# Kernel optimization log

Measured on AMD Instinct MI355X. Metric: run time of the kernel, lower is better.

## Reference

```python
import jax, jax.numpy as jnp
import numpy as np

B, N = 32, 128
V, P, L = 50000, 40, 50
WD, UD = 100, 25
D = WD + UD          # 125: LSTM hidden per direction
H2 = 2 * D           # 250: BiLSTM output
HID = 100            # hidden_dim for scorers


def setup_inputs() -> dict:
    key = jax.random.key(0)
    ks = iter(jax.random.split(key, 40))
    p = lambda shape: jax.random.normal(next(ks), shape, jnp.float32) * 0.05
    inp = {
        'word_ids': jax.random.randint(next(ks), (B, N), 0, V),
        'upos_ids': jax.random.randint(next(ks), (B, N), 0, P),
        'target_arcs': jax.random.randint(next(ks), (B, N), 0, N),
        'wlookup': p((V, WD)),
        'tlookup': p((V, UD)),  # original sizes tag table by word_count
        # LSTM layer 0 (input D=125), layer 1 (input 2D=250); f=fwd, b=bwd dir
        'l0f_Wih': p((4 * D, D)), 'l0f_Whh': p((4 * D, D)), 'l0f_b': p((4 * D,)),
        'l0b_Wih': p((4 * D, D)), 'l0b_Whh': p((4 * D, D)), 'l0b_b': p((4 * D,)),
        'l1f_Wih': p((4 * D, H2)), 'l1f_Whh': p((4 * D, D)), 'l1f_b': p((4 * D,)),
        'l1b_Wih': p((4 * D, H2)), 'l1b_Whh': p((4 * D, D)), 'l1b_b': p((4 * D,)),
        'eh_W': p((HID, H2)), 'eh_b': p((HID,)),
        'em_W': p((HID, H2)), 'em_b': p((HID,)),
        'es_W': p((1, HID)), 'es_b': p((1,)),
        'lh_W': p((HID, H2)), 'lh_b': p((HID,)),
        'lm_W': p((HID, H2)), 'lm_b': p((HID,)),
        'ls_W': p((L, HID)), 'ls_b': p((L,)),
    }
    return inp


def _lstm_dir(x, Wih, Whh, b, reverse):
    # x: [B,T,in] -> h: [B,T,H], pytorch gate order i,f,g,o
    H = Whh.shape[1]
    xg = jnp.einsum('bti,gi->btg', x, Wih) + b  # precompute input projections

    def step(carry, xt):
        h, c = carry
        g = xt + h @ Whh.T
        i, f, gg, o = jnp.split(g, 4, axis=-1)
        c = jax.nn.sigmoid(f) * c + jax.nn.sigmoid(i) * jnp.tanh(gg)
        h = jax.nn.sigmoid(o) * jnp.tanh(c)
        return (h, c), h

    h0 = jnp.zeros((x.shape[0], H), x.dtype)
    _, hs = jax.lax.scan(step, (h0, h0), jnp.swapaxes(xg, 0, 1), reverse=reverse)
    return jnp.swapaxes(hs, 0, 1)


def _bilstm(x, Wf, Uf, bf, Wb, Ub, bb):
    return jnp.concatenate([_lstm_dir(x, Wf, Uf, bf, False),
                            _lstm_dir(x, Wb, Ub, bb, True)], axis=-1)


def reference(word_ids, upos_ids, target_arcs, wlookup, tlookup,
              l0f_Wih, l0f_Whh, l0f_b, l0b_Wih, l0b_Whh, l0b_b,
              l1f_Wih, l1f_Whh, l1f_b, l1b_Wih, l1b_Whh, l1b_b,
              eh_W, eh_b, em_W, em_b, es_W, es_b,
              lh_W, lh_b, lm_W, lm_b, ls_W, ls_b):
    n = word_ids.shape[1]
    words = jnp.concatenate([wlookup[word_ids], tlookup[upos_ids]], axis=-1)  # [B,N,125]
    h0 = _bilstm(words, l0f_Wih, l0f_Whh, l0f_b, l0b_Wih, l0b_Whh, l0b_b)
    word_exprs = _bilstm(h0, l1f_Wih, l1f_Whh, l1f_b, l1b_Wih, l1b_Whh, l1b_b)  # [B,N,250]

    word_h = word_exprs @ eh_W.T + eh_b  # [B,N,100]
    word_m = word_exprs @ em_W.T + em_b
    # fused pairwise biaffine-style scoring (replaces the O(n) python loop)
    pair = jnp.tanh(word_h[:, :, None, :] + word_m[:, None, :, :])  # [B,N,N,100]
    arc_scores = jnp.einsum('bijh,h->bij', pair, es_W[0]) + es_b[0]  # [B,N,N]

    # training path: margin augmentation
    target_arcs = target_arcs.at[:, 0].set(0)
    margin = 1.0 - jax.nn.one_hot(target_arcs, n, dtype=arc_scores.dtype)
    arc_scores = arc_scores + margin

    # decode() is an external MST decoder; greedy argmax stand-in
    parsed_trees = jnp.argmax(arc_scores, axis=-1)

    tree = target_arcs  # is_train path
    rel_heads = jnp.take_along_axis(word_exprs, tree[:, :, None], axis=1)  # [B,N,250]
    rel_heads = rel_heads @ lh_W.T + lh_b
    rel_mod = word_exprs @ lm_W.T + lm_b
    rel_scores = jnp.tanh(rel_mod + rel_heads) @ ls_W.T + ls_b  # [B,N,L]
    predicted_rels = jnp.argmax(rel_scores, axis=-1)
    return (parsed_trees, predicted_rels, arc_scores, rel_scores)
```

## Files before the change

kernel.cpp:

```cpp
#include <hip/hip_runtime.h>
#include <hip/hip_bf16.h>
#include <math.h>

#define B 32
#define N 128
#define BT (B*N)
#define WD 100
#define UD 25
#define D 125
#define G4 (4*D)
#define H2 (2*D)
#define HID 100
#define L 50

__device__ __forceinline__ float fast_tanh(float x) {
    float e = __expf(2.0f * x);
    return 1.0f - 2.0f / (e + 1.0f);
}
__device__ __forceinline__ float fast_sigmoid(float x) {
    return 1.0f / (1.0f + __expf(-x));
}
__device__ __forceinline__ float bcast_lane(float v, int k) {
    return __builtin_bit_cast(float, __builtin_amdgcn_readlane(__builtin_bit_cast(int, v), k));
}

#define REP64(X) \
 X(0) X(1) X(2) X(3) X(4) X(5) X(6) X(7) X(8) X(9) \
 X(10) X(11) X(12) X(13) X(14) X(15) X(16) X(17) X(18) X(19) \
 X(20) X(21) X(22) X(23) X(24) X(25) X(26) X(27) X(28) X(29) \
 X(30) X(31) X(32) X(33) X(34) X(35) X(36) X(37) X(38) X(39) \
 X(40) X(41) X(42) X(43) X(44) X(45) X(46) X(47) X(48) X(49) \
 X(50) X(51) X(52) X(53) X(54) X(55) X(56) X(57) X(58) X(59) \
 X(60) X(61) X(62) X(63)

__global__ void bias_setup(const float* __restrict__ l0f_b, const float* __restrict__ l0b_b,
                           const float* __restrict__ l1f_b, const float* __restrict__ l1b_b,
                           const float* __restrict__ eh_b, const float* __restrict__ em_b,
                           const float* __restrict__ lm_b,
                           float* __restrict__ b_l0, float* __restrict__ b_l1,
                           float* __restrict__ b_s3) {
    int t = blockIdx.x * blockDim.x + threadIdx.x;
    if (t < 500)        b_l0[t] = l0f_b[t];
    else if (t < 1000)  b_l0[t] = l0b_b[t-500];
    else if (t < 1500)  b_l1[t-1000] = l1f_b[t-1000];
    else if (t < 2000)  b_l1[t-1000] = l1b_b[t-1500];
    else if (t < 2100)  b_s3[t-2000] = eh_b[t-2000];
    else if (t < 2200)  b_s3[t-2000] = em_b[t-2100];
    else if (t < 2300)  b_s3[t-2000] = lm_b[t-2200];
}

__global__ void pad_zero(float* __restrict__ w0, float* __restrict__ w1,
                         float* __restrict__ w2, float* __restrict__ w3) {
    int t = blockIdx.x * blockDim.x + threadIdx.x;
    int m = t / 1516, e = t % 1516;
    float* p = (m == 0) ? w0 : (m == 1) ? w1 : (m == 2) ? w2 : w3;
    p[125*500 + e] = 0.0f;
}

struct TJob { const float* src; float* dst; int R, C, ldo, coff, tile0, tiles_x; };
struct TArgs { TJob j[12]; };

__global__ __launch_bounds__(256)
void transpose_fused(TArgs a) {
    int bid = blockIdx.x;
    int ji = 0;
    #pragma unroll
    for (int i = 1; i < 12; i++) if (bid >= a.j[i].tile0) ji = i;
    TJob jb = a.j[ji];
    int t = bid - jb.tile0;
    int tx = t % jb.tiles_x;
    int ty = t / jb.tiles_x;
    __shared__ float tile[32][33];
    int k0 = tx*32, n0 = ty*32;
    #pragma unroll
    for (int dy = 0; dy < 32; dy += 8) {
        int n = n0 + threadIdx.y + dy;
        int k = k0 + threadIdx.x;
        if (n < jb.R && k < jb.C)
            tile[threadIdx.y+dy][threadIdx.x] = jb.src[(size_t)n*jb.C + k];
    }
    __syncthreads();
    #pragma unroll
    for (int dy = 0; dy < 32; dy += 8) {
        int k = k0 + threadIdx.y + dy;
        int n = n0 + threadIdx.x;
        if (k < jb.C && n < jb.R)
            jb.dst[(size_t)k*jb.ldo + jb.coff + n] = tile[threadIdx.x][threadIdx.y+dy];
    }
}

__global__ void embed_kernel(const int* __restrict__ wids, const int* __restrict__ uids,
                             const float* __restrict__ wl, const float* __restrict__ tl,
                             float* __restrict__ words) {
    int bt = blockIdx.x;
    int t = threadIdx.x;
    int wid = wids[bt];
    int uid = uids[bt];
    if (t < WD)       words[bt*D + t] = wl[wid*WD + t];
    else if (t < D)   words[bt*D + t] = tl[uid*UD + (t - WD)];
}

#define MT 16
template<int CPT>
__global__ __launch_bounds__(512)
void proj_t(const float* __restrict__ x, const float* __restrict__ WT,
            const float* __restrict__ bias, float* __restrict__ out,
            int Ncols, int K, int ldx, const int* __restrict__ gather_idx) {
    __shared__ float xs[250 * 17 + 16];
    int m0 = blockIdx.x * MT;
    for (int e = threadIdx.x; e < MT * K; e += blockDim.x) {
        int r = e / K, k = e - r * K;
        int m = m0 + r;
        int row = m;
        if (gather_idx) {
            int bb = m >> 7, np = m & 127;
            row = (bb << 7) + (np == 0 ? 0 : gather_idx[m]);
        }
        xs[k*17 + r] = x[(size_t)row*ldx + k];
    }
    __syncthreads();
    int n0 = threadIdx.x;
    int lane = threadIdx.x & 63;
    int bd = blockDim.x;
    float acc[CPT][MT];
    int ncl[CPT];
    #pragma unroll
    for (int j = 0; j < CPT; j++) {
        int n = n0 + j*bd;
        ncl[j] = (n < Ncols) ? n : (Ncols - 1);
        #pragma unroll
        for (int r = 0; r < MT; r++) acc[j][r] = 0.0f;
    }
    float wkc[4][CPT];
    #pragma unroll
    for (int q = 0; q < 4; q++)
        #pragma unroll
        for (int j = 0; j < CPT; j++)
            wkc[q][j] = WT[(size_t)q*Ncols + ncl[j]];
    int k0 = 0;
    for (; k0 + 8 <= K; k0 += 4) {
        float xv = xs[(k0 + (lane >> 4))*17 + (lane & 15)];
        float wkn[4][CPT];
        #pragma unroll
        for (int q = 0; q < 4; q++)
            #pragma unroll
            for (int j = 0; j < CPT; j++)
                wkn[q][j] = WT[(size_t)(k0 + 4 + q)*Ncols + ncl[j]];
        #pragma unroll
        for (int q = 0; q < 4; q++) {
            #pragma unroll
            for (int r = 0; r < 16; r++) {
                float hv = bcast_lane(xv, q*16 + r);
                #pragma unroll
                for (int j = 0; j < CPT; j++)
                    acc[j][r] = fmaf(wkc[q][j], hv, acc[j][r]);
            }
        }
        #pragma unroll
        for (int q = 0; q < 4; q++)
            #pragma unroll
            for (int j = 0; j < CPT; j++)
                wkc[q][j] = wkn[q][j];
    }
    {
        float xv = xs[(k0 + (lane >> 4))*17 + (lane & 15)];
        #pragma unroll
        for (int q = 0; q < 4; q++) {
            #pragma unroll
            for (int r = 0; r < 16; r++) {
                float hv = bcast_lane(xv, q*16 + r);
                #pragma unroll
                for (int j = 0; j < CPT; j++)
                    acc[j][r] = fmaf(wkc[q][j], hv, acc[j][r]);
            }
        }
        k0 += 4;
    }
    for (; k0 < K; k0++) {
        float xv = xs[k0*17 + (lane & 15)];
        float wk[CPT];
        #pragma unroll
        for (int j = 0; j < CPT; j++) wk[j] = WT[(size_t)k0*Ncols + ncl[j]];
        #pragma unroll
        for (int r = 0; r < 16; r++) {
            float hv = bcast_lane(xv, r);
            #pragma unroll
            for (int j = 0; j < CPT; j++)
                acc[j][r] = fmaf(wk[j], hv, acc[j][r]);
        }
    }
    #pragma unroll
    for (int j = 0; j < CPT; j++) {
        int n = n0 + j*bd;
        if (n < Ncols) {
            float bb = bias[n];
            #pragma unroll
            for (int r = 0; r < MT; r++) out[(size_t)(m0 + r)*Ncols + n] = acc[j][r] + bb;
        }
    }
}

__global__ __launch_bounds__(1024, 4)
void lstm_scan(const float* __restrict__ xgc,
               const float* __restrict__ WhTf, const float* __restrict__ WhTb,
               float* __restrict__ out) {
    int dir = blockIdx.x & 1;
    int b = blockIdx.x >> 1;
    const float* WhT = dir ? WhTb : WhTf;
    int off = dir ? D : 0;
    int t = threadIdx.x;
    int g = t & 511;
    int half = t >> 9;
    int kbase = half << 6;

    __shared__ __align__(16) float hbuf[128];
    __shared__ float pbuf[1024];

    unsigned voff0 = ((unsigned)kbase * 500u + (unsigned)g) * 4u;
#define DECLW(i) float w##i; \
    asm volatile("global_load_dword %0, %1, %2" \
                 : "=v"(w##i) : "v"(voff0 + (unsigned)(i)*2000u), "s"(WhT));
    REP64(DECLW)
#undef DECLW
    asm volatile("s_waitcnt vmcnt(0)" ::: "memory");

    float c = 0.0f;
    if (t < 128) hbuf[t] = 0.0f;
    __syncthreads();

    const float* xb = xgc + (size_t)b * N * 1000 + dir * 500;
    bool xa = (half == 0) && (g < G4);
    float x_next = xa ? xb[(size_t)(dir ? (N-1) : 0) * 1000 + g] : 0.0f;

    const float4* h4q = ((const float4*)hbuf) + (kbase >> 2);

#define FMA4(q, i0, i1, i2, i3) { float4 hv = h4q[q]; \
    a4[0] = fmaf(w##i0, hv.x, a4[0]); \
    a4[1] = fmaf(w##i1, hv.y, a4[1]); \
    a4[2] = fmaf(w##i2, hv.z, a4[2]); \
    a4[3] = fmaf(w##i3, hv.w, a4[3]); }

    for (int ti = 0; ti < N; ti++) {
        int tt = dir ? (N-1-ti) : ti;
        float x_cur = x_next;
        float xn = 0.0f;
        if (xa && ti + 1 < N)
            xn = xb[(size_t)(dir ? (tt-1) : (tt+1)) * 1000 + g];
        float a4[4];
        a4[0] = x_cur; a4[1] = 0.0f; a4[2] = 0.0f; a4[3] = 0.0f;
        FMA4(0,  0,  1,  2,  3)  FMA4(1,  4,  5,  6,  7)
        FMA4(2,  8,  9, 10, 11)  FMA4(3, 12, 13, 14, 15)
        FMA4(4, 16, 17, 18, 19)  FMA4(5, 20, 21, 22, 23)
        FMA4(6, 24, 25, 26, 27)  FMA4(7, 28, 29, 30, 31)
        FMA4(8, 32, 33, 34, 35)  FMA4(9, 36, 37, 38, 39)
        FMA4(10, 40, 41, 42, 43) FMA4(11, 44, 45, 46, 47)
        FMA4(12, 48, 49, 50, 51) FMA4(13, 52, 53, 54, 55)
        FMA4(14, 56, 57, 58, 59) FMA4(15, 60, 61, 62, 63)
        x_next = xn;
        pbuf[t] = (a4[0] + a4[1]) + (a4[2] + a4[3]);
        __syncthreads();
        if (t < D) {
            float iv = pbuf[t]       + pbuf[512 + t];
            float fv = pbuf[D+t]     + pbuf[512 + D+t];
            float gv = pbuf[2*D+t]   + pbuf[512 + 2*D+t];
            float ov = pbuf[3*D+t]   + pbuf[512 + 3*D+t];
            float si = fast_sigmoid(iv);
            float sf = fast_sigmoid(fv);
            float so = fast_sigmoid(ov);
            c = sf * c + si * fast_tanh(gv);
            float h = so * fast_tanh(c);
            hbuf[t] = h;
            out[(size_t)(b*N + tt)*H2 + off + t] = h;
        }
        __syncthreads();
    }
#undef FMA4
}

#define ITILE 4
__global__ __launch_bounds__(128)
void arc_kernel(const float* __restrict__ s3,
                const float* __restrict__ esW, const float* __restrict__ esb,
                const int* __restrict__ ta,
                float* __restrict__ arc_out, float* __restrict__ tree_out) {
    int blk = blockIdx.x;
    int b = blk >> 5, it = blk & 31;
    int j = threadIdx.x;

    __shared__ float wms[128 * 101];
    __shared__ float whs[ITILE][HID];
    __shared__ float es[HID];
    __shared__ float sv[128];
    __shared__ int   si[128];

    for (int e = j; e < 128 * HID; e += 128) {
        int r = e / HID, h = e - r * HID;
        wms[r*101 + h] = s3[(size_t)(b*N + r)*300 + 100 + h];
    }
    for (int e = j; e < ITILE * HID; e += 128) {
        int ii = e / HID, h = e - ii * HID;
        whs[ii][h] = s3[(size_t)(b*N + it*ITILE + ii)*300 + h];
    }
    if (j < HID) es[j] = esW[j];
    __syncthreads();

    float eb = esb[0];
    const float* wmr = &wms[j * 101];
    for (int ii = 0; ii < ITILE; ii++) {
        int i = it * ITILE + ii;
        int bi = b * N + i;
        float acc = 0.0f;
        for (int h = 0; h < HID; h++)
            acc = fmaf(es[h], fast_tanh(whs[ii][h] + wmr[h]), acc);
        int tai = (i == 0) ? 0 : ta[bi];
        float score = acc + eb + 1.0f - ((j == tai) ? 1.0f : 0.0f);
        arc_out[(size_t)bi*N + j] = score;
        sv[j] = score; si[j] = j;
        __syncthreads();
        for (int s = 64; s; s >>= 1) {
            if (j < s) {
                float ov = sv[j+s]; int oi = si[j+s];
                if (ov > sv[j] || (ov == sv[j] && oi < si[j])) { sv[j] = ov; si[j] = oi; }
            }
            __syncthreads();
        }
        if (j == 0) tree_out[bi] = (float)si[0];
        __syncthreads();
    }
}

__global__ void rel_kernel(const float* __restrict__ s3, const float* __restrict__ rh,
                           const float* __restrict__ lsW, const float* __restrict__ lsb,
                           float* __restrict__ rel_out, float* __restrict__ pred_out) {
    int bt = blockIdx.x;
    int t = threadIdx.x;

    __shared__ float tv[HID];
    __shared__ float sv[64];
    __shared__ int   si[64];

    for (int h = t; h < HID; h += 64)
        tv[h] = fast_tanh(s3[(size_t)bt*300 + 200 + h] + rh[(size_t)bt*HID + h]);
    __syncthreads();

    float score = -1e30f;
    if (t < L) {
        float acc = 0.0f;
        const float* wrow = lsW + t*HID;
        for (int h = 0; h < HID; h++) acc = fmaf(wrow[h], tv[h], acc);
        score = acc + lsb[t];
        rel_out[(size_t)bt*L + t] = score;
    }
    sv[t] = score;
    si[t] = t;
    __syncthreads();
    for (int s = 32; s; s >>= 1) {
        if (t < s) {
            float ov = sv[t + s]; int oi = si[t + s];
            if (ov > sv[t] || (ov == sv[t] && oi < si[t])) { sv[t] = ov; si[t] = oi; }
        }
        __syncthreads();
    }
    if (t == 0) pred_out[bt] = (float)si[0];
}

extern "C" void kernel_launch(void* const* d_in, const int* in_sizes, int n_in,
                              void* d_out, int out_size, void* d_ws, size_t ws_size,
                              hipStream_t stream) {
    const int*   word_ids    = (const int*)  d_in[0];
    const int*   upos_ids    = (const int*)  d_in[1];
    const int*   target_arcs = (const int*)  d_in[2];
    const float* wlookup     = (const float*)d_in[3];
    const float* tlookup     = (const float*)d_in[4];
    const float* l0f_Wih = (const float*)d_in[5];
    const float* l0f_Whh = (const float*)d_in[6];
    const float* l0f_b   = (const float*)d_in[7];
    const float* l0b_Wih = (const float*)d_in[8];
    const float* l0b_Whh = (const float*)d_in[9];
    const float* l0b_b   = (const float*)d_in[10];
    const float* l1f_Wih = (const float*)d_in[11];
    const float* l1f_Whh = (const float*)d_in[12];
    const float* l1f_b   = (const float*)d_in[13];
    const float* l1b_Wih = (const float*)d_in[14];
    const float* l1b_Whh = (const float*)d_in[15];
    const float* l1b_b   = (const float*)d_in[16];
    const float* eh_W = (const float*)d_in[17];
    const float* eh_b = (const float*)d_in[18];
    const float* em_W = (const float*)d_in[19];
    const float* em_b = (const float*)d_in[20];
    const float* es_W = (const float*)d_in[21];
    const float* es_b = (const float*)d_in[22];
    const float* lh_W = (const float*)d_in[23];
    const float* lh_b = (const float*)d_in[24];
    const float* lm_W = (const float*)d_in[25];
    const float* lm_b = (const float*)d_in[26];
    const float* ls_W = (const float*)d_in[27];
    const float* ls_b = (const float*)d_in[28];

    float* out = (float*)d_out;
    float* trees_out = out;
    float* preds_out = out + BT;
    float* arc_out   = out + 2*BT;
    float* rel_out   = out + 2*BT + BT*N;

    float* ws = (float*)d_ws;
    float* A       = ws;
    float* words   = ws + 4096000;
    float* C       = ws + 4608000;
    float* WT_l0   = ws + 5632000;
    float* WT_l1   = ws + 5757000;
    float* WT_s3   = ws + 6007000;
    float* WT_lh   = ws + 6082000;
    float* WhT_l0f = ws + 6107000;
    float* WhT_l0b = ws + 6171016;
    float* WhT_l1f = ws + 6235032;
    float* WhT_l1b = ws + 6299048;
    float* b_l0    = ws + 6363064;
    float* b_l1    = ws + 6364064;
    float* b_s3    = ws + 6365064;
    float* rel_head = ws + 6366064;

    bias_setup<<<9, 256, 0, stream>>>(l0f_b, l0b_b, l1f_b, l1b_b, eh_b, em_b, lm_b,
                                      b_l0, b_l1, b_s3);
    pad_zero<<<24, 256, 0, stream>>>(WhT_l0f, WhT_l0b, WhT_l1f, WhT_l1b);
    {
        TArgs ta{};
        auto tiles = [](int R, int C_) { return ((C_+31)/32) * ((R+31)/32); };
        struct { const float* s; float* d; int R, C, ldo, coff; } js[12] = {
            { l0f_Wih, WT_l0, 500, 125, 1000, 0 },
            { l0b_Wih, WT_l0, 500, 125, 1000, 500 },
            { l1f_Wih, WT_l1, 500, 250, 1000, 0 },
            { l1b_Wih, WT_l1, 500, 250, 1000, 500 },
            { eh_W, WT_s3, 100, 250, 300, 0 },
            { em_W, WT_s3, 100, 250, 300, 100 },
            { lm_W, WT_s3, 100, 250, 300, 200 },
            { lh_W, WT_lh, 100, 250, 100, 0 },
            { l0f_Whh, WhT_l0f, 500, 125, 500, 0 },
            { l0b_Whh, WhT_l0b, 500, 125, 500, 0 },
            { l1f_Whh, WhT_l1f, 500, 125, 500, 0 },
            { l1b_Whh, WhT_l1b, 500, 125, 500, 0 },
        };
        int t0 = 0;
        for (int i = 0; i < 12; i++) {
            ta.j[i].src = js[i].s;  ta.j[i].dst = js[i].d;
            ta.j[i].R = js[i].R;    ta.j[i].C = js[i].C;
            ta.j[i].ldo = js[i].ldo; ta.j[i].coff = js[i].coff;
            ta.j[i].tile0 = t0;
            ta.j[i].tiles_x = (js[i].C + 31) / 32;
            t0 += tiles(js[i].R, js[i].C);
        }
        transpose_fused<<<t0, dim3(32, 8), 0, stream>>>(ta);
    }

    embed_kernel<<<BT, 128, 0, stream>>>(word_ids, upos_ids, wlookup, tlookup, words);

    proj_t<2><<<BT/MT, 512, 0, stream>>>(words, WT_l0, b_l0, A, 1000, D, D, nullptr);

    lstm_scan<<<B*2, 1024, 0, stream>>>(A, WhT_l0f, WhT_l0b, C);

    proj_t<2><<<BT/MT, 512, 0, stream>>>(C, WT_l1, b_l1, A, 1000, H2, H2, nullptr);

    lstm_scan<<<B*2, 1024, 0, stream>>>(A, WhT_l1f, WhT_l1b, C);

    proj_t<2><<<BT/MT, 192, 0, stream>>>(C, WT_s3, b_s3, A, 300, H2, H2, nullptr);
    proj_t<1><<<BT/MT, 128, 0, stream>>>(C, WT_lh, lh_b, rel_head, 100, H2, H2, target_arcs);

    arc_kernel<<<BT/ITILE, 128, 0, stream>>>(A, es_W, es_b, target_arcs,
                                             arc_out, trees_out);

    rel_kernel<<<BT, 64, 0, stream>>>(A, rel_head, ls_W, ls_b, rel_out, preds_out);
}
```

Measured before the change: 627.8 us.

## Merge setup, projection, and scoring kernels to cut launch count

Folds bias copy, padding, weight transposes and embedding gather into one setup kernel. Merges the two final projections into one launch, and the arc and rel scoring kernels into another, using block-index dispatch. This goes from 11 launches to 6, removing launch gaps and tail effects. In exchange, the merged projections now use 256 threads with a fixed CPT of 2 (before: 192 and 128 threads), which shifts occupancy and wastes threads on the 100-column job.

Measured after the change: 593.3 us. 5.5% less time.

```diff
diff --git a/kernel.cpp b/kernel.cpp
--- a/kernel.cpp
+++ b/kernel.cpp
@@ -33,82 +33,88 @@
  X(50) X(51) X(52) X(53) X(54) X(55) X(56) X(57) X(58) X(59) \
  X(60) X(61) X(62) X(63)
 
-__global__ void bias_setup(const float* __restrict__ l0f_b, const float* __restrict__ l0b_b,
-                           const float* __restrict__ l1f_b, const float* __restrict__ l1b_b,
-                           const float* __restrict__ eh_b, const float* __restrict__ em_b,
-                           const float* __restrict__ lm_b,
-                           float* __restrict__ b_l0, float* __restrict__ b_l1,
-                           float* __restrict__ b_s3) {
-    int t = blockIdx.x * blockDim.x + threadIdx.x;
-    if (t < 500)        b_l0[t] = l0f_b[t];
-    else if (t < 1000)  b_l0[t] = l0b_b[t-500];
-    else if (t < 1500)  b_l1[t-1000] = l1f_b[t-1000];
-    else if (t < 2000)  b_l1[t-1000] = l1b_b[t-1500];
-    else if (t < 2100)  b_s3[t-2000] = eh_b[t-2000];
-    else if (t < 2200)  b_s3[t-2000] = em_b[t-2100];
-    else if (t < 2300)  b_s3[t-2000] = lm_b[t-2200];
-}
-
-__global__ void pad_zero(float* __restrict__ w0, float* __restrict__ w1,
-                         float* __restrict__ w2, float* __restrict__ w3) {
-    int t = blockIdx.x * blockDim.x + threadIdx.x;
-    int m = t / 1516, e = t % 1516;
-    float* p = (m == 0) ? w0 : (m == 1) ? w1 : (m == 2) ? w2 : w3;
-    p[125*500 + e] = 0.0f;
-}
-
 struct TJob { const float* src; float* dst; int R, C, ldo, coff, tile0, tiles_x; };
 struct TArgs { TJob j[12]; };
 
 __global__ __launch_bounds__(256)
-void transpose_fused(TArgs a) {
+void setup_fused(TArgs a, int n_tr,
+                 const int* __restrict__ wids, const int* __restrict__ uids,
+                 const float* __restrict__ wl, const float* __restrict__ tl,
+                 float* __restrict__ words,
+                 const float* __restrict__ l0f_b, const float* __restrict__ l0b_b,
+                 const float* __restrict__ l1f_b, const float* __restrict__ l1b_b,
+                 const float* __restrict__ eh_b, const float* __restrict__ em_b,
+                 const float* __restrict__ lm_b,
+                 float* __restrict__ b_l0, float* __restrict__ b_l1,
+                 float* __restrict__ b_s3,
+                 float* __restrict__ p0, float* __restrict__ p1,
+                 float* __restrict__ p2, float* __restrict__ p3) {
+    __shared__ float tile[32][33];
     int bid = blockIdx.x;
-    int ji = 0;
-    #pragma unroll
-    for (int i = 1; i < 12; i++) if (bid >= a.j[i].tile0) ji = i;
-    TJob jb = a.j[ji];
-    int t = bid - jb.tile0;
-    int tx = t % jb.tiles_x;
-    int ty = t / jb.tiles_x;
-    __shared__ float tile[32][33];
-    int k0 = tx*32, n0 = ty*32;
-    #pragma unroll
-    for (int dy = 0; dy < 32; dy += 8) {
-        int n = n0 + threadIdx.y + dy;
-        int k = k0 + threadIdx.x;
-        if (n < jb.R && k < jb.C)
-            tile[threadIdx.y+dy][threadIdx.x] = jb.src[(size_t)n*jb.C + k];
-    }
-    __syncthreads();
-    #pragma unroll
-    for (int dy = 0; dy < 32; dy += 8) {
-        int k = k0 + threadIdx.y + dy;
-        int n = n0 + threadIdx.x;
-        if (k < jb.C && n < jb.R)
-            jb.dst[(size_t)k*jb.ldo + jb.coff + n] = tile[threadIdx.x][threadIdx.y+dy];
-    }
-}
-
-__global__ void embed_kernel(const int* __restrict__ wids, const int* __restrict__ uids,
-                             const float* __restrict__ wl, const float* __restrict__ tl,
-                             float* __restrict__ words) {
-    int bt = blockIdx.x;
-    int t = threadIdx.x;
-    int wid = wids[bt];
-    int uid = uids[bt];
-    if (t < WD)       words[bt*D + t] = wl[wid*WD + t];
-    else if (t < D)   words[bt*D + t] = tl[uid*UD + (t - WD)];
+    int tid = threadIdx.x;
+    if (bid < n_tr) {
+        int ji = 0;
+        #pragma unroll
+        for (int i = 1; i < 12; i++) if (bid >= a.j[i].tile0) ji = i;
+        TJob jb = a.j[ji];
+        int t = bid - jb.tile0;
+        int tx = t % jb.tiles_x, ty = t / jb.tiles_x;
+        int txx = tid & 31, tyy = tid >> 5;
+        int k0 = tx*32, n0 = ty*32;
+        #pragma unroll
+        for (int dy = 0; dy < 32; dy += 8) {
+            int n = n0 + tyy + dy, k = k0 + txx;
+            if (n < jb.R && k < jb.C)
+                tile[tyy+dy][txx] = jb.src[(size_t)n*jb.C + k];
+        }
+        __syncthreads();
+        #pragma unroll
+        for (int dy = 0; dy < 32; dy += 8) {
+            int k = k0 + tyy + dy, n = n0 + txx;
+            if (k < jb.C && n < jb.R)
+                jb.dst[(size_t)k*jb.ldo + jb.coff + n] = tile[txx][tyy+dy];
+        }
+        return;
+    }
+    bid -= n_tr;
+    if (bid < 2048) {
+        int bt = bid*2 + (tid >> 7);
+        int t = tid & 127;
+        int wid = wids[bt], uid = uids[bt];
+        if (t < WD)       words[bt*D + t] = wl[(size_t)wid*WD + t];
+        else if (t < D)   words[bt*D + t] = tl[(size_t)uid*UD + (t - WD)];
+        return;
+    }
+    bid -= 2048;
+    if (bid < 9) {
+        int t = bid*256 + tid;
+        if (t < 500)        b_l0[t] = l0f_b[t];
+        else if (t < 1000)  b_l0[t] = l0b_b[t-500];
+        else if (t < 1500)  b_l1[t-1000] = l1f_b[t-1000];
+        else if (t < 2000)  b_l1[t-1000] = l1b_b[t-1500];
+        else if (t < 2100)  b_s3[t-2000] = eh_b[t-2000];
+        else if (t < 2200)  b_s3[t-2000] = em_b[t-2100];
+        else if (t < 2300)  b_s3[t-2000] = lm_b[t-2200];
+        return;
+    }
+    bid -= 9;
+    int e = bid*256 + tid;
+    if (e < 6064) {
+        int m = e / 1516, o = e % 1516;
+        float* p = (m == 0) ? p0 : (m == 1) ? p1 : (m == 2) ? p2 : p3;
+        p[125*500 + o] = 0.0f;
+    }
 }
 
 #define MT 16
-template<int CPT>
-__global__ __launch_bounds__(512)
-void proj_t(const float* __restrict__ x, const float* __restrict__ WT,
-            const float* __restrict__ bias, float* __restrict__ out,
-            int Ncols, int K, int ldx, const int* __restrict__ gather_idx) {
-    __shared__ float xs[250 * 17 + 16];
-    int m0 = blockIdx.x * MT;
-    for (int e = threadIdx.x; e < MT * K; e += blockDim.x) {
+template<int CPT, int BD>
+__device__ __forceinline__
+void proj_body(const float* __restrict__ x, const float* __restrict__ WT,
+               const float* __restrict__ bias, float* __restrict__ out,
+               int Ncols, int K, int ldx, const int* __restrict__ gather_idx,
+               int blk, float* xs) {
+    int m0 = blk * MT;
+    for (int e = threadIdx.x; e < MT * K; e += BD) {
         int r = e / K, k = e - r * K;
         int m = m0 + r;
         int row = m;
@@ -121,12 +127,11 @@
     __syncthreads();
     int n0 = threadIdx.x;
     int lane = threadIdx.x & 63;
-    int bd = blockDim.x;
     float acc[CPT][MT];
     int ncl[CPT];
     #pragma unroll
     for (int j = 0; j < CPT; j++) {
-        int n = n0 + j*bd;
+        int n = n0 + j*BD;
         ncl[j] = (n < Ncols) ? n : (Ncols - 1);
         #pragma unroll
         for (int r = 0; r < MT; r++) acc[j][r] = 0.0f;
@@ -191,13 +196,36 @@
     }
     #pragma unroll
     for (int j = 0; j < CPT; j++) {
-        int n = n0 + j*bd;
+        int n = n0 + j*BD;
         if (n < Ncols) {
             float bb = bias[n];
             #pragma unroll
             for (int r = 0; r < MT; r++) out[(size_t)(m0 + r)*Ncols + n] = acc[j][r] + bb;
         }
     }
+}
+
+__global__ __launch_bounds__(512)
+void proj_t(const float* __restrict__ x, const float* __restrict__ WT,
+            const float* __restrict__ bias, float* __restrict__ out,
+            int Ncols, int K, int ldx) {
+    __shared__ float xs[250 * 17 + 16];
+    proj_body<2, 512>(x, WT, bias, out, Ncols, K, ldx, nullptr, blockIdx.x, xs);
+}
+
+__global__ __launch_bounds__(256)
+void proj_s3lh(const float* __restrict__ x,
+               const float* __restrict__ WTa, const float* __restrict__ ba,
+               float* __restrict__ outa,
+               const float* __restrict__ WTb, const float* __restrict__ bb,
+               float* __restrict__ outb, const int* __restrict__ gather_idx) {
+    __shared__ float xs[250 * 17 + 16];
+    int job = blockIdx.x >> 8;
+    int blk = blockIdx.x & 255;
+    if (job == 0)
+        proj_body<2, 256>(x, WTa, ba, outa, 300, H2, H2, nullptr, blk, xs);
+    else
+        proj_body<2, 256>(x, WTb, bb, outb, 100, H2, H2, gather_idx, blk, xs);
 }
 
 __global__ __launch_bounds__(1024, 4)
@@ -279,42 +307,69 @@
 
 #define ITILE 4
 __global__ __launch_bounds__(128)
-void arc_kernel(const float* __restrict__ s3,
-                const float* __restrict__ esW, const float* __restrict__ esb,
-                const int* __restrict__ ta,
-                float* __restrict__ arc_out, float* __restrict__ tree_out) {
-    int blk = blockIdx.x;
-    int b = blk >> 5, it = blk & 31;
-    int j = threadIdx.x;
-
+void arc_rel(const float* __restrict__ s3,
+             const float* __restrict__ esW, const float* __restrict__ esb,
+             const int* __restrict__ ta, const float* __restrict__ rh,
+             const float* __restrict__ lsW, const float* __restrict__ lsb,
+             float* __restrict__ arc_out, float* __restrict__ tree_out,
+             float* __restrict__ rel_out, float* __restrict__ pred_out) {
     __shared__ float wms[128 * 101];
     __shared__ float whs[ITILE][HID];
     __shared__ float es[HID];
     __shared__ float sv[128];
     __shared__ int   si[128];
-
-    for (int e = j; e < 128 * HID; e += 128) {
-        int r = e / HID, h = e - r * HID;
-        wms[r*101 + h] = s3[(size_t)(b*N + r)*300 + 100 + h];
-    }
-    for (int e = j; e < ITILE * HID; e += 128) {
-        int ii = e / HID, h = e - ii * HID;
-        whs[ii][h] = s3[(size_t)(b*N + it*ITILE + ii)*300 + h];
-    }
-    if (j < HID) es[j] = esW[j];
-    __syncthreads();
-
-    float eb = esb[0];
-    const float* wmr = &wms[j * 101];
-    for (int ii = 0; ii < ITILE; ii++) {
-        int i = it * ITILE + ii;
-        int bi = b * N + i;
-        float acc = 0.0f;
-        for (int h = 0; h < HID; h++)
-            acc = fmaf(es[h], fast_tanh(whs[ii][h] + wmr[h]), acc);
-        int tai = (i == 0) ? 0 : ta[bi];
-        float score = acc + eb + 1.0f - ((j == tai) ? 1.0f : 0.0f);
-        arc_out[(size_t)bi*N + j] = score;
+    int j = threadIdx.x;
+
+    if (blockIdx.x < 1024) {
+        int blk = blockIdx.x;
+        int b = blk >> 5, it = blk & 31;
+        for (int e = j; e < 128 * HID; e += 128) {
+            int r = e / HID, h = e - r * HID;
+            wms[r*101 + h] = s3[(size_t)(b*N + r)*300 + 100 + h];
+        }
+        for (int e = j; e < ITILE * HID; e += 128) {
+            int ii = e / HID, h = e - ii * HID;
+            whs[ii][h] = s3[(size_t)(b*N + it*ITILE + ii)*300 + h];
+        }
+        if (j < HID) es[j] = esW[j];
+        __syncthreads();
+        float eb = esb[0];
+        const float* wmr = &wms[j * 101];
+        for (int ii = 0; ii < ITILE; ii++) {
+            int i = it * ITILE + ii;
+            int bi = b * N + i;
+            float acc = 0.0f;
+            for (int h = 0; h < HID; h++)
+                acc = fmaf(es[h], fast_tanh(whs[ii][h] + wmr[h]), acc);
+            int tai = (i == 0) ? 0 : ta[bi];
+            float score = acc + eb + 1.0f - ((j == tai) ? 1.0f : 0.0f);
+            arc_out[(size_t)bi*N + j] = score;
+            sv[j] = score; si[j] = j;
+            __syncthreads();
+            for (int s = 64; s; s >>= 1) {
+                if (j < s) {
+                    float ov = sv[j+s]; int oi = si[j+s];
+                    if (ov > sv[j] || (ov == sv[j] && oi < si[j])) { sv[j] = ov; si[j] = oi; }
+                }
+                __syncthreads();
+            }
+            if (j == 0) tree_out[bi] = (float)si[0];
+            __syncthreads();
+        }
+    } else {
+        int bt = blockIdx.x - 1024;
+        float* tv = es;
+        if (j < HID)
+            tv[j] = fast_tanh(s3[(size_t)bt*300 + 200 + j] + rh[(size_t)bt*HID + j]);
+        __syncthreads();
+        float score = -1e30f;
+        if (j < L) {
+            float acc = 0.0f;
+            const float* wrow = lsW + j*HID;
+            for (int h = 0; h < HID; h++) acc = fmaf(wrow[h], tv[h], acc);
+            score = acc + lsb[j];
+            rel_out[(size_t)bt*L + j] = score;
+        }
         sv[j] = score; si[j] = j;
         __syncthreads();
         for (int s = 64; s; s >>= 1) {
@@ -324,44 +379,8 @@
             }
             __syncthreads();
         }
-        if (j == 0) tree_out[bi] = (float)si[0];
-        __syncthreads();
-    }
-}
-
-__global__ void rel_kernel(const float* __restrict__ s3, const float* __restrict__ rh,
-                           const float* __restrict__ lsW, const float* __restrict__ lsb,
-                           float* __restrict__ rel_out, float* __restrict__ pred_out) {
-    int bt = blockIdx.x;
-    int t = threadIdx.x;
-
-    __shared__ float tv[HID];
-    __shared__ float sv[64];
-    __shared__ int   si[64];
-
-    for (int h = t; h < HID; h += 64)
-        tv[h] = fast_tanh(s3[(size_t)bt*300 + 200 + h] + rh[(size_t)bt*HID + h]);
-    __syncthreads();
-
-    float score = -1e30f;
-    if (t < L) {
-        float acc = 0.0f;
-        const float* wrow = lsW + t*HID;
-        for (int h = 0; h < HID; h++) acc = fmaf(wrow[h], tv[h], acc);
-        score = acc + lsb[t];
-        rel_out[(size_t)bt*L + t] = score;
-    }
-    sv[t] = score;
-    si[t] = t;
-    __syncthreads();
-    for (int s = 32; s; s >>= 1) {
-        if (t < s) {
-            float ov = sv[t + s]; int oi = si[t + s];
-            if (ov > sv[t] || (ov == sv[t] && oi < si[t])) { sv[t] = ov; si[t] = oi; }
-        }
-        __syncthreads();
-    }
-    if (t == 0) pred_out[bt] = (float)si[0];
+        if (j == 0) pred_out[bt] = (float)si[0];
+    }
 }
 
 extern "C" void kernel_launch(void* const* d_in, const int* in_sizes, int n_in,
@@ -420,11 +439,9 @@
     float* b_s3    = ws + 6365064;
     float* rel_head = ws + 6366064;
 
-    bias_setup<<<9, 256, 0, stream>>>(l0f_b, l0b_b, l1f_b, l1b_b, eh_b, em_b, lm_b,
-                                      b_l0, b_l1, b_s3);
-    pad_zero<<<24, 256, 0, stream>>>(WhT_l0f, WhT_l0b, WhT_l1f, WhT_l1b);
+    TArgs ta{};
+    int n_tr = 0;
     {
-        TArgs ta{};
         auto tiles = [](int R, int C_) { return ((C_+31)/32) * ((R+31)/32); };
         struct { const float* s; float* d; int R, C, ldo, coff; } js[12] = {
             { l0f_Wih, WT_l0, 500, 125, 1000, 0 },
@@ -440,33 +457,32 @@
             { l1f_Whh, WhT_l1f, 500, 125, 500, 0 },
             { l1b_Whh, WhT_l1b, 500, 125, 500, 0 },
         };
-        int t0 = 0;
         for (int i = 0; i < 12; i++) {
             ta.j[i].src = js[i].s;  ta.j[i].dst = js[i].d;
             ta.j[i].R = js[i].R;    ta.j[i].C = js[i].C;
             ta.j[i].ldo = js[i].ldo; ta.j[i].coff = js[i].coff;
-            ta.j[i].tile0 = t0;
+            ta.j[i].tile0 = n_tr;
             ta.j[i].tiles_x = (js[i].C + 31) / 32;
-            t0 += tiles(js[i].R, js[i].C);
-        }
-        transpose_fused<<<t0, dim3(32, 8), 0, stream>>>(ta);
-    }
-
-    embed_kernel<<<BT, 128, 0, stream>>>(word_ids, upos_ids, wlookup, tlookup, words);
-
-    proj_t<2><<<BT/MT, 512, 0, stream>>>(words, WT_l0, b_l0, A, 1000, D, D, nullptr);
+            n_tr += tiles(js[i].R, js[i].C);
+        }
+    }
+    setup_fused<<<n_tr + 2048 + 9 + 24, 256, 0, stream>>>(
+        ta, n_tr, word_ids, upos_ids, wlookup, tlookup, words,
+        l0f_b, l0b_b, l1f_b, l1b_b, eh_b, em_b, lm_b,
+        b_l0, b_l1, b_s3, WhT_l0f, WhT_l0b, WhT_l1f, WhT_l1b);
+
+    proj_t<<<BT/MT, 512, 0, stream>>>(words, WT_l0, b_l0, A, 1000, D, D);
 
     lstm_scan<<<B*2, 1024, 0, stream>>>(A, WhT_l0f, WhT_l0b, C);
 
-    proj_t<2><<<BT/MT, 512, 0, stream>>>(C, WT_l1, b_l1, A, 1000, H2, H2, nullptr);
+    proj_t<<<BT/MT, 512, 0, stream>>>(C, WT_l1, b_l1, A, 1000, H2, H2);
 
     lstm_scan<<<B*2, 1024, 0, stream>>>(A, WhT_l1f, WhT_l1b, C);
 
-    proj_t<2><<<BT/MT, 192, 0, stream>>>(C, WT_s3, b_s3, A, 300, H2, H2, nullptr);
-    proj_t<1><<<BT/MT, 128, 0, stream>>>(C, WT_lh, lh_b, rel_head, 100, H2, H2, target_arcs);
-
-    arc_kernel<<<BT/ITILE, 128, 0, stream>>>(A, es_W, es_b, target_arcs,
-                                             arc_out, trees_out);
-
-    rel_kernel<<<BT, 64, 0, stream>>>(A, rel_head, ls_W, ls_b, rel_out, preds_out);
-}
+    proj_s3lh<<<512, 256, 0, stream>>>(C, WT_s3, b_s3, A,
+                                       WT_lh, lh_b, rel_head, target_arcs);
+
+    arc_rel<<<1024 + BT, 128, 0, stream>>>(A, es_W, es_b, target_arcs, rel_head,
+                                           ls_W, ls_b, arc_out, trees_out,
+                                           rel_out, preds_out);
+}
```

## Fuse all stages into one cooperative persistent kernel with grid syncs

Applied to the files above, without the earlier changes.

Replaces the sequence of separate launches (setup, transpose, embed, projections, two LSTM scans, arc and rel scoring) with a single cooperative kernel of 256 blocks of 1024 threads. Stages are separated by grid.sync(). The goal is to remove per-launch overhead and the gaps between kernels. The weight transpose becomes a naive strided copy without a shared-memory tile. The arc and rel argmax reductions now use wave shuffles. In exchange, the projection stages run at fixed 1024-thread blocks with half the threads idle. The LSTM scan stages use only 64 of the 256 blocks, and grid-wide barriers add their own latency.

New measurement: 786.8 us. 25.3% more time.

```diff
diff --git a/kernel.cpp b/kernel.cpp
--- a/kernel.cpp
+++ b/kernel.cpp
@@ -1,6 +1,9 @@
 #include <hip/hip_runtime.h>
 #include <hip/hip_bf16.h>
+#include <hip/hip_cooperative_groups.h>
 #include <math.h>
+
+namespace cg = cooperative_groups;
 
 #define B 32
 #define N 128
@@ -12,6 +15,7 @@
 #define H2 (2*D)
 #define HID 100
 #define L 50
+#define MT 16
 
 __device__ __forceinline__ float fast_tanh(float x) {
     float e = __expf(2.0f * x);
@@ -33,82 +37,24 @@
  X(50) X(51) X(52) X(53) X(54) X(55) X(56) X(57) X(58) X(59) \
  X(60) X(61) X(62) X(63)
 
-__global__ void bias_setup(const float* __restrict__ l0f_b, const float* __restrict__ l0b_b,
-                           const float* __restrict__ l1f_b, const float* __restrict__ l1b_b,
-                           const float* __restrict__ eh_b, const float* __restrict__ em_b,
-                           const float* __restrict__ lm_b,
-                           float* __restrict__ b_l0, float* __restrict__ b_l1,
-                           float* __restrict__ b_s3) {
-    int t = blockIdx.x * blockDim.x + threadIdx.x;
-    if (t < 500)        b_l0[t] = l0f_b[t];
-    else if (t < 1000)  b_l0[t] = l0b_b[t-500];
-    else if (t < 1500)  b_l1[t-1000] = l1f_b[t-1000];
-    else if (t < 2000)  b_l1[t-1000] = l1b_b[t-1500];
-    else if (t < 2100)  b_s3[t-2000] = eh_b[t-2000];
-    else if (t < 2200)  b_s3[t-2000] = em_b[t-2100];
-    else if (t < 2300)  b_s3[t-2000] = lm_b[t-2200];
-}
-
-__global__ void pad_zero(float* __restrict__ w0, float* __restrict__ w1,
-                         float* __restrict__ w2, float* __restrict__ w3) {
-    int t = blockIdx.x * blockDim.x + threadIdx.x;
-    int m = t / 1516, e = t % 1516;
-    float* p = (m == 0) ? w0 : (m == 1) ? w1 : (m == 2) ? w2 : w3;
-    p[125*500 + e] = 0.0f;
-}
-
-struct TJob { const float* src; float* dst; int R, C, ldo, coff, tile0, tiles_x; };
-struct TArgs { TJob j[12]; };
-
-__global__ __launch_bounds__(256)
-void transpose_fused(TArgs a) {
-    int bid = blockIdx.x;
-    int ji = 0;
-    #pragma unroll
-    for (int i = 1; i < 12; i++) if (bid >= a.j[i].tile0) ji = i;
-    TJob jb = a.j[ji];
-    int t = bid - jb.tile0;
-    int tx = t % jb.tiles_x;
-    int ty = t / jb.tiles_x;
-    __shared__ float tile[32][33];
-    int k0 = tx*32, n0 = ty*32;
-    #pragma unroll
-    for (int dy = 0; dy < 32; dy += 8) {
-        int n = n0 + threadIdx.y + dy;
-        int k = k0 + threadIdx.x;
-        if (n < jb.R && k < jb.C)
-            tile[threadIdx.y+dy][threadIdx.x] = jb.src[(size_t)n*jb.C + k];
-    }
-    __syncthreads();
-    #pragma unroll
-    for (int dy = 0; dy < 32; dy += 8) {
-        int k = k0 + threadIdx.y + dy;
-        int n = n0 + threadIdx.x;
-        if (k < jb.C && n < jb.R)
-            jb.dst[(size_t)k*jb.ldo + jb.coff + n] = tile[threadIdx.x][threadIdx.y+dy];
-    }
-}
-
-__global__ void embed_kernel(const int* __restrict__ wids, const int* __restrict__ uids,
-                             const float* __restrict__ wl, const float* __restrict__ tl,
-                             float* __restrict__ words) {
-    int bt = blockIdx.x;
-    int t = threadIdx.x;
-    int wid = wids[bt];
-    int uid = uids[bt];
-    if (t < WD)       words[bt*D + t] = wl[wid*WD + t];
-    else if (t < D)   words[bt*D + t] = tl[uid*UD + (t - WD)];
-}
-
-#define MT 16
-template<int CPT>
-__global__ __launch_bounds__(512)
-void proj_t(const float* __restrict__ x, const float* __restrict__ WT,
-            const float* __restrict__ bias, float* __restrict__ out,
-            int Ncols, int K, int ldx, const int* __restrict__ gather_idx) {
-    __shared__ float xs[250 * 17 + 16];
-    int m0 = blockIdx.x * MT;
-    for (int e = threadIdx.x; e < MT * K; e += blockDim.x) {
+struct TJob { const float* src; float* dst; int R, C, ldo, coff; };
+
+struct KArgs {
+    const int *wids, *uids, *tarcs;
+    const float *wl, *tl;
+    const float *l0f_b, *l0b_b, *l1f_b, *l1b_b, *eh_b, *em_b, *lm_b, *lh_b;
+    const float *esW, *esb, *lsW, *lsb;
+    TJob j[12];
+    float *A, *words, *C, *WT_l0, *WT_l1, *WT_s3, *WT_lh;
+    float *WhT_l0f, *WhT_l0b, *WhT_l1f, *WhT_l1b;
+    float *b_l0, *b_l1, *b_s3, *rel_head;
+    float *trees, *preds, *arc, *rel;
+};
+
+__device__ __forceinline__
+void proj_stage(int tid, int nthr, const float* __restrict__ x, int K, int ldx,
+                const int* __restrict__ gather_idx, int m0, float* xs) {
+    for (int e = tid; e < MT * K; e += nthr) {
         int r = e / K, k = e - r * K;
         int m = m0 + r;
         int row = m;
@@ -118,15 +64,19 @@
         }
         xs[k*17 + r] = x[(size_t)row*ldx + k];
     }
-    __syncthreads();
-    int n0 = threadIdx.x;
-    int lane = threadIdx.x & 63;
-    int bd = blockDim.x;
+}
+
+template<int CPT, int BD>
+__device__ __forceinline__
+void proj_compute(int tid, const float* xs, const float* __restrict__ WT,
+                  const float* __restrict__ bias, float* __restrict__ out,
+                  int Ncols, int K, int m0) {
+    int lane = tid & 63;
     float acc[CPT][MT];
     int ncl[CPT];
     #pragma unroll
     for (int j = 0; j < CPT; j++) {
-        int n = n0 + j*bd;
+        int n = tid + j*BD;
         ncl[j] = (n < Ncols) ? n : (Ncols - 1);
         #pragma unroll
         for (int r = 0; r < MT; r++) acc[j][r] = 0.0f;
@@ -191,7 +141,7 @@
     }
     #pragma unroll
     for (int j = 0; j < CPT; j++) {
-        int n = n0 + j*bd;
+        int n = tid + j*BD;
         if (n < Ncols) {
             float bb = bias[n];
             #pragma unroll
@@ -200,21 +150,18 @@
     }
 }
 
-__global__ __launch_bounds__(1024, 4)
-void lstm_scan(const float* __restrict__ xgc,
+__device__ __forceinline__
+void scan_body(int blk, const float* __restrict__ xgc,
                const float* __restrict__ WhTf, const float* __restrict__ WhTb,
-               float* __restrict__ out) {
-    int dir = blockIdx.x & 1;
-    int b = blockIdx.x >> 1;
+               float* __restrict__ out, float* hbuf, float* pbuf) {
+    int dir = blk & 1;
+    int b = blk >> 1;
     const float* WhT = dir ? WhTb : WhTf;
     int off = dir ? D : 0;
     int t = threadIdx.x;
     int g = t & 511;
     int half = t >> 9;
     int kbase = half << 6;
-
-    __shared__ __align__(16) float hbuf[128];
-    __shared__ float pbuf[1024];
 
     unsigned voff0 = ((unsigned)kbase * 500u + (unsigned)g) * 4u;
 #define DECLW(i) float w##i; \
@@ -277,91 +224,166 @@
 #undef FMA4
 }
 
-#define ITILE 4
-__global__ __launch_bounds__(128)
-void arc_kernel(const float* __restrict__ s3,
-                const float* __restrict__ esW, const float* __restrict__ esb,
-                const int* __restrict__ ta,
-                float* __restrict__ arc_out, float* __restrict__ tree_out) {
+__device__ __forceinline__ void amax_step(float& v, int& i, float vo, int io) {
+    if (vo > v || (vo == v && io < i)) { v = vo; i = io; }
+}
+
+__global__ __launch_bounds__(1024)
+void mega_kernel(KArgs a) {
+    cg::grid_group grid = cg::this_grid();
+    __shared__ __align__(16) float smem[14720];
+    int tid = threadIdx.x;
     int blk = blockIdx.x;
-    int b = blk >> 5, it = blk & 31;
-    int j = threadIdx.x;
-
-    __shared__ float wms[128 * 101];
-    __shared__ float whs[ITILE][HID];
-    __shared__ float es[HID];
-    __shared__ float sv[128];
-    __shared__ int   si[128];
-
-    for (int e = j; e < 128 * HID; e += 128) {
-        int r = e / HID, h = e - r * HID;
-        wms[r*101 + h] = s3[(size_t)(b*N + r)*300 + 100 + h];
-    }
-    for (int e = j; e < ITILE * HID; e += 128) {
-        int ii = e / HID, h = e - ii * HID;
-        whs[ii][h] = s3[(size_t)(b*N + it*ITILE + ii)*300 + h];
-    }
-    if (j < HID) es[j] = esW[j];
-    __syncthreads();
-
-    float eb = esb[0];
-    const float* wmr = &wms[j * 101];
-    for (int ii = 0; ii < ITILE; ii++) {
-        int i = it * ITILE + ii;
-        int bi = b * N + i;
-        float acc = 0.0f;
-        for (int h = 0; h < HID; h++)
-            acc = fmaf(es[h], fast_tanh(whs[ii][h] + wmr[h]), acc);
-        int tai = (i == 0) ? 0 : ta[bi];
-        float score = acc + eb + 1.0f - ((j == tai) ? 1.0f : 0.0f);
-        arc_out[(size_t)bi*N + j] = score;
-        sv[j] = score; si[j] = j;
-        __syncthreads();
-        for (int s = 64; s; s >>= 1) {
-            if (j < s) {
-                float ov = sv[j+s]; int oi = si[j+s];
-                if (ov > sv[j] || (ov == sv[j] && oi < si[j])) { sv[j] = ov; si[j] = oi; }
+    size_t gstride = (size_t)gridDim.x * blockDim.x;
+    size_t gtid = (size_t)blk * blockDim.x + tid;
+
+    for (int ji = 0; ji < 12; ji++) {
+        TJob jb = a.j[ji];
+        int tot = jb.R * jb.C;
+        for (size_t e = gtid; e < (size_t)tot; e += gstride) {
+            int n = (int)(e / jb.C), k = (int)(e - (size_t)n*jb.C);
+            jb.dst[(size_t)k*jb.ldo + jb.coff + n] = jb.src[e];
+        }
+    }
+    for (size_t e = gtid; e < (size_t)BT*D; e += gstride) {
+        int bt = (int)(e / D), t = (int)(e - (size_t)bt*D);
+        a.words[e] = (t < WD) ? a.wl[(size_t)a.wids[bt]*WD + t]
+                              : a.tl[(size_t)a.uids[bt]*UD + (t - WD)];
+    }
+    for (size_t e = gtid; e < 2300; e += gstride) {
+        int t = (int)e;
+        if (t < 500)        a.b_l0[t] = a.l0f_b[t];
+        else if (t < 1000)  a.b_l0[t] = a.l0b_b[t-500];
+        else if (t < 1500)  a.b_l1[t-1000] = a.l1f_b[t-1000];
+        else if (t < 2000)  a.b_l1[t-1000] = a.l1b_b[t-1500];
+        else if (t < 2100)  a.b_s3[t-2000] = a.eh_b[t-2000];
+        else if (t < 2200)  a.b_s3[t-2000] = a.em_b[t-2100];
+        else                a.b_s3[t-2000] = a.lm_b[t-2200];
+    }
+    for (size_t e = gtid; e < 4*1516; e += gstride) {
+        int m = (int)(e / 1516), o = (int)(e % 1516);
+        float* p = (m == 0) ? a.WhT_l0f : (m == 1) ? a.WhT_l0b
+                 : (m == 2) ? a.WhT_l1f : a.WhT_l1b;
+        p[125*500 + o] = 0.0f;
+    }
+    grid.sync();
+
+    {
+        int m0 = blk * MT;
+        proj_stage(tid, 1024, a.words, D, D, nullptr, m0, smem);
+        __syncthreads();
+        if (tid < 512)
+            proj_compute<2, 512>(tid, smem, a.WT_l0, a.b_l0, a.A, 1000, D, m0);
+    }
+    grid.sync();
+
+    if (blk < 64) scan_body(blk, a.A, a.WhT_l0f, a.WhT_l0b, a.C, smem, smem + 128);
+    grid.sync();
+
+    {
+        int m0 = blk * MT;
+        proj_stage(tid, 1024, a.C, H2, H2, nullptr, m0, smem);
+        __syncthreads();
+        if (tid < 512)
+            proj_compute<2, 512>(tid, smem, a.WT_l1, a.b_l1, a.A, 1000, H2, m0);
+    }
+    grid.sync();
+
+    if (blk < 64) scan_body(blk, a.A, a.WhT_l1f, a.WhT_l1b, a.C, smem, smem + 128);
+    grid.sync();
+
+    {
+        int m0 = blk * MT;
+        float* xs1 = smem;
+        float* xs2 = smem + 4272;
+        if (tid < 512) proj_stage(tid, 512, a.C, H2, H2, nullptr, m0, xs1);
+        else           proj_stage(tid - 512, 512, a.C, H2, H2, a.tarcs, m0, xs2);
+        __syncthreads();
+        if (tid < 512) {
+            if ((tid & ~63) < 300)
+                proj_compute<1, 512>(tid, xs1, a.WT_s3, a.b_s3, a.A, 300, H2, m0);
+        } else {
+            int t2 = tid - 512;
+            if ((t2 & ~63) < 100)
+                proj_compute<1, 512>(t2, xs2, a.WT_lh, a.lh_b, a.rel_head, 100, H2, m0);
+        }
+    }
+    grid.sync();
+
+    {
+        float* wms  = smem;
+        float* whs  = smem + 12928;
+        float* es   = smem + 14528;
+        float* redv = smem + 14628;
+        int*   redi = (int*)(smem + 14644);
+
+        int b = blk >> 3;
+        int ig0 = (blk & 7) * 16;
+        for (int e = tid; e < 128 * HID; e += 1024) {
+            int r = e / HID, h = e - r * HID;
+            wms[r*101 + h] = a.A[(size_t)(b*N + r)*300 + 100 + h];
+        }
+        for (int e = tid; e < 16 * HID; e += 1024) {
+            int ii = e / HID, h = e - ii * HID;
+            whs[e] = a.A[(size_t)(b*N + ig0 + ii)*300 + h];
+        }
+        if (tid < HID) es[tid] = a.esW[tid];
+        __syncthreads();
+
+        float eb = a.esb[0];
+        int j = tid & 127;
+        int sub = tid >> 7;
+        const float* wmr = &wms[j * 101];
+        for (int iter = 0; iter < 2; iter++) {
+            int ii = sub + iter*8;
+            int i = ig0 + ii;
+            int bi = b * N + i;
+            float acc = 0.0f;
+            const float* whr = &whs[ii * HID];
+            for (int h = 0; h < HID; h++)
+                acc = fmaf(es[h], fast_tanh(whr[h] + wmr[h]), acc);
+            int tai = (i == 0) ? 0 : a.tarcs[bi];
+            float score = acc + eb + 1.0f - ((j == tai) ? 1.0f : 0.0f);
+            a.arc[(size_t)bi*N + j] = score;
+            float v = score; int vi = j;
+            #pragma unroll
+            for (int off = 32; off; off >>= 1)
+                amax_step(v, vi, __shfl_down(v, off), __shfl_down(vi, off));
+            if ((tid & 63) == 0) {
+                int w = tid >> 6;
+                redv[w] = v; redi[w] = vi;
             }
             __syncthreads();
-        }
-        if (j == 0) tree_out[bi] = (float)si[0];
-        __syncthreads();
-    }
-}
-
-__global__ void rel_kernel(const float* __restrict__ s3, const float* __restrict__ rh,
-                           const float* __restrict__ lsW, const float* __restrict__ lsb,
-                           float* __restrict__ rel_out, float* __restrict__ pred_out) {
-    int bt = blockIdx.x;
-    int t = threadIdx.x;
-
-    __shared__ float tv[HID];
-    __shared__ float sv[64];
-    __shared__ int   si[64];
-
-    for (int h = t; h < HID; h += 64)
-        tv[h] = fast_tanh(s3[(size_t)bt*300 + 200 + h] + rh[(size_t)bt*HID + h]);
-    __syncthreads();
-
-    float score = -1e30f;
-    if (t < L) {
-        float acc = 0.0f;
-        const float* wrow = lsW + t*HID;
-        for (int h = 0; h < HID; h++) acc = fmaf(wrow[h], tv[h], acc);
-        score = acc + lsb[t];
-        rel_out[(size_t)bt*L + t] = score;
-    }
-    sv[t] = score;
-    si[t] = t;
-    __syncthreads();
-    for (int s = 32; s; s >>= 1) {
-        if (t < s) {
-            float ov = sv[t + s]; int oi = si[t + s];
-            if (ov > sv[t] || (ov == sv[t] && oi < si[t])) { sv[t] = ov; si[t] = oi; }
-        }
-        __syncthreads();
-    }
-    if (t == 0) pred_out[bt] = (float)si[0];
+            if (j == 0) {
+                float v0 = redv[sub*2], v1 = redv[sub*2+1];
+                int  i0 = redi[sub*2], i1 = redi[sub*2+1];
+                amax_step(v0, i0, v1, i1);
+                a.trees[bi] = (float)i0;
+            }
+            __syncthreads();
+        }
+
+        __syncthreads();
+        int grp = tid >> 6, t = tid & 63;
+        int bt = blk * 16 + grp;
+        float* tv = smem + grp * 104;
+        for (int h = t; h < HID; h += 64)
+            tv[h] = fast_tanh(a.A[(size_t)bt*300 + 200 + h] + a.rel_head[(size_t)bt*HID + h]);
+        __syncthreads();
+        float score = -1e30f;
+        if (t < L) {
+            float acc = 0.0f;
+            const float* wrow = a.lsW + t*HID;
+            for (int h = 0; h < HID; h++) acc = fmaf(wrow[h], tv[h], acc);
+            score = acc + a.lsb[t];
+            a.rel[(size_t)bt*L + t] = score;
+        }
+        float v = score; int vi = t;
+        #pragma unroll
+        for (int off = 32; off; off >>= 1)
+            amax_step(v, vi, __shfl_down(v, off), __shfl_down(vi, off));
+        if (t == 0) a.preds[bt] = (float)vi;
+    }
 }
 
 extern "C" void kernel_launch(void* const* d_in, const int* in_sizes, int n_in,
@@ -398,75 +420,53 @@
     const float* ls_b = (const float*)d_in[28];
 
     float* out = (float*)d_out;
-    float* trees_out = out;
-    float* preds_out = out + BT;
-    float* arc_out   = out + 2*BT;
-    float* rel_out   = out + 2*BT + BT*N;
-
     float* ws = (float*)d_ws;
-    float* A       = ws;
-    float* words   = ws + 4096000;
-    float* C       = ws + 4608000;
-    float* WT_l0   = ws + 5632000;
-    float* WT_l1   = ws + 5757000;
-    float* WT_s3   = ws + 6007000;
-    float* WT_lh   = ws + 6082000;
-    float* WhT_l0f = ws + 6107000;
-    float* WhT_l0b = ws + 6171016;
-    float* WhT_l1f = ws + 6235032;
-    float* WhT_l1b = ws + 6299048;
-    float* b_l0    = ws + 6363064;
-    float* b_l1    = ws + 6364064;
-    float* b_s3    = ws + 6365064;
-    float* rel_head = ws + 6366064;
-
-    bias_setup<<<9, 256, 0, stream>>>(l0f_b, l0b_b, l1f_b, l1b_b, eh_b, em_b, lm_b,
-                                      b_l0, b_l1, b_s3);
-    pad_zero<<<24, 256, 0, stream>>>(WhT_l0f, WhT_l0b, WhT_l1f, WhT_l1b);
-    {
-        TArgs ta{};
-        auto tiles = [](int R, int C_) { return ((C_+31)/32) * ((R+31)/32); };
-        struct { const float* s; float* d; int R, C, ldo, coff; } js[12] = {
-            { l0f_Wih, WT_l0, 500, 125, 1000, 0 },
-            { l0b_Wih, WT_l0, 500, 125, 1000, 500 },
-            { l1f_Wih, WT_l1, 500, 250, 1000, 0 },
-            { l1b_Wih, WT_l1, 500, 250, 1000, 500 },
-            { eh_W, WT_s3, 100, 250, 300, 0 },
-            { em_W, WT_s3, 100, 250, 300, 100 },
-            { lm_W, WT_s3, 100, 250, 300, 200 },
-            { lh_W, WT_lh, 100, 250, 100, 0 },
-            { l0f_Whh, WhT_l0f, 500, 125, 500, 0 },
-            { l0b_Whh, WhT_l0b, 500, 125, 500, 0 },
-            { l1f_Whh, WhT_l1f, 500, 125, 500, 0 },
-            { l1b_Whh, WhT_l1b, 500, 125, 500, 0 },
-        };
-        int t0 = 0;
-        for (int i = 0; i < 12; i++) {
-            ta.j[i].src = js[i].s;  ta.j[i].dst = js[i].d;
-            ta.j[i].R = js[i].R;    ta.j[i].C = js[i].C;
-            ta.j[i].ldo = js[i].ldo; ta.j[i].coff = js[i].coff;
-            ta.j[i].tile0 = t0;
-            ta.j[i].tiles_x = (js[i].C + 31) / 32;
-            t0 += tiles(js[i].R, js[i].C);
-        }
-        transpose_fused<<<t0, dim3(32, 8), 0, stream>>>(ta);
-    }
-
-    embed_kernel<<<BT, 128, 0, stream>>>(word_ids, upos_ids, wlookup, tlookup, words);
-
-    proj_t<2><<<BT/MT, 512, 0, stream>>>(words, WT_l0, b_l0, A, 1000, D, D, nullptr);
-
-    lstm_scan<<<B*2, 1024, 0, stream>>>(A, WhT_l0f, WhT_l0b, C);
-
-    proj_t<2><<<BT/MT, 512, 0, stream>>>(C, WT_l1, b_l1, A, 1000, H2, H2, nullptr);
-
-    lstm_scan<<<B*2, 1024, 0, stream>>>(A, WhT_l1f, WhT_l1b, C);
-
-    proj_t<2><<<BT/MT, 192, 0, stream>>>(C, WT_s3, b_s3, A, 300, H2, H2, nullptr);
-    proj_t<1><<<BT/MT, 128, 0, stream>>>(C, WT_lh, lh_b, rel_head, 100, H2, H2, target_arcs);
-
-    arc_kernel<<<BT/ITILE, 128, 0, stream>>>(A, es_W, es_b, target_arcs,
-                                             arc_out, trees_out);
-
-    rel_kernel<<<BT, 64, 0, stream>>>(A, rel_head, ls_W, ls_b, rel_out, preds_out);
-}
+
+    KArgs ka{};
+    ka.wids = word_ids; ka.uids = upos_ids; ka.tarcs = target_arcs;
+    ka.wl = wlookup; ka.tl = tlookup;
+    ka.l0f_b = l0f_b; ka.l0b_b = l0b_b; ka.l1f_b = l1f_b; ka.l1b_b = l1b_b;
+    ka.eh_b = eh_b; ka.em_b = em_b; ka.lm_b = lm_b; ka.lh_b = lh_b;
+    ka.esW = es_W; ka.esb = es_b; ka.lsW = ls_W; ka.lsb = ls_b;
+
+    ka.A       = ws;
+    ka.words   = ws + 4096000;
+    ka.C       = ws + 4608000;
+    ka.WT_l0   = ws + 5632000;
+    ka.WT_l1   = ws + 5757000;
+    ka.WT_s3   = ws + 6007000;
+    ka.WT_lh   = ws + 6082000;
+    ka.WhT_l0f = ws + 6107000;
+    ka.WhT_l0b = ws + 6171016;
+    ka.WhT_l1f = ws + 6235032;
+    ka.WhT_l1b = ws + 6299048;
+    ka.b_l0    = ws + 6363064;
+    ka.b_l1    = ws + 6364064;
+    ka.b_s3    = ws + 6365064;
+    ka.rel_head = ws + 6366064;
+
+    ka.trees = out;
+    ka.preds = out + BT;
+    ka.arc   = out + 2*BT;
+    ka.rel   = out + 2*BT + BT*N;
+
+    TJob js[12] = {
+        { l0f_Wih, ka.WT_l0, 500, 125, 1000, 0 },
+        { l0b_Wih, ka.WT_l0, 500, 125, 1000, 500 },
+        { l1f_Wih, ka.WT_l1, 500, 250, 1000, 0 },
+        { l1b_Wih, ka.WT_l1, 500, 250, 1000, 500 },
+        { eh_W, ka.WT_s3, 100, 250, 300, 0 },
+        { em_W, ka.WT_s3, 100, 250, 300, 100 },
+        { lm_W, ka.WT_s3, 100, 250, 300, 200 },
+        { lh_W, ka.WT_lh, 100, 250, 100, 0 },
+        { l0f_Whh, ka.WhT_l0f, 500, 125, 500, 0 },
+        { l0b_Whh, ka.WhT_l0b, 500, 125, 500, 0 },
+        { l1f_Whh, ka.WhT_l1f, 500, 125, 500, 0 },
+        { l1b_Whh, ka.WhT_l1b, 500, 125, 500, 0 },
+    };
+    for (int i = 0; i < 12; i++) ka.j[i] = js[i];
+
+    void* params[] = { &ka };
+    hipLaunchCooperativeKernel((const void*)mega_kernel, dim3(256), dim3(1024),
+                               params, 0, stream);
+}
```
